# Optimization experiments

Measured on AMD Instinct MI355X. Metric: run time of the kernel, lower is better.

Reference implementation:

```python
import jax, jax.numpy as jnp
import numpy as np

B, M, D = 64, 256, 256          # batch, tokens, feature dim
A = 18                          # num_actions
E, S = 4, 64                    # num_experts, slots per expert (E*S == M)
H = 512                         # expert hidden size


def setup_inputs() -> dict:
    key = jax.random.key(0)
    ks = jax.random.split(key, 7)
    obs = jax.random.normal(ks[0], (B, M, D), dtype=jnp.float32)
    action = jax.random.randint(ks[1], (B,), 0, A, dtype=jnp.int64)
    # Soft-MoE slot projection phi: [D, E, S]
    phi = jax.random.normal(ks[2], (D, E, S), dtype=jnp.float32) / np.sqrt(D)
    # Per-expert MLP: Dense(H) + relu, then Dense(A*D) output head
    w1 = jax.random.normal(ks[3], (E, D, H), dtype=jnp.float32) * np.sqrt(2.0 / D)
    b1 = jnp.zeros((E, H), dtype=jnp.float32)
    w2 = jax.random.normal(ks[4], (E, H, A * D), dtype=jnp.float32) * np.sqrt(2.0 / H)
    b2 = jnp.zeros((E, A * D), dtype=jnp.float32)
    return {"obs": obs, "action": action, "phi": phi,
            "w1": w1, "b1": b1, "w2": w2, "b2": b2}


def reference(obs, action, phi, w1, b1, w2, b2):
    b, m, d = obs.shape
    # ---- Soft-MoE dispatch / combine (Puigcerver et al.) ----
    logits = jnp.einsum('bmd,des->bmes', obs, phi)            # [b,m,e,s]
    dispatch = jax.nn.softmax(logits, axis=1)                 # softmax over tokens
    combine = jax.nn.softmax(logits.reshape(b, m, E * S), axis=-1)
    combine = combine.reshape(b, m, E, S)                     # softmax over all slots
    slots = jnp.einsum('bmd,bmes->besd', obs, dispatch)       # [b,e,s,d]
    # ---- per-expert MLP: Dense(H)+relu -> Dense(A*d) ----
    h = jax.nn.relu(jnp.einsum('besd,edh->besh', slots, w1) + b1[None, :, None, :])
    y = jnp.einsum('besh,ehk->besk', h, w2) + b2[None, :, None, :]   # k = A*d
    # ---- combine slots back to tokens ----
    out = jnp.einsum('bmes,besk->bmk', combine, y)            # [b,m,A*d]
    # reshape to [b, A, m, d] as in the original module
    out = out.reshape(b, m, A, d).transpose(0, 2, 1, 3)       # [b,A,m,d]
    # ---- one-hot action selection via einsum (as in source) ----
    action_one_hot = jax.nn.one_hot(action, A, dtype=out.dtype)
    logits_out = jnp.einsum('bamd,ba->bmd', out, action_one_hot)
    return logits_out  # logits of the categorical transition distribution
```

## Files before the change

### kernel.cpp

```cpp
#include <hip/hip_runtime.h>

#define B_   64
#define M_   256
#define D_   256
#define A_   18
#define E_   4
#define S_   64
#define ES_  256
#define H_   512
#define K2_  (A_*D_)

typedef _Float16 f16;
typedef _Float16 f16x4 __attribute__((ext_vector_type(4)));
typedef _Float16 f16x8 __attribute__((ext_vector_type(8)));
typedef float    f32x4 __attribute__((ext_vector_type(4)));

static __device__ __forceinline__ f16x8 cat8(f16x4 a, f16x4 b) {
  return __builtin_shufflevector(a, b, 0, 1, 2, 3, 4, 5, 6, 7);
}
static __device__ __forceinline__ f16x8 pack8(float4 u0, float4 u1) {
  f16x8 a;
  a[0] = (f16)u0.x; a[1] = (f16)u0.y; a[2] = (f16)u0.z; a[3] = (f16)u0.w;
  a[4] = (f16)u1.x; a[5] = (f16)u1.y; a[6] = (f16)u1.z; a[7] = (f16)u1.w;
  return a;
}

typedef const __attribute__((address_space(1))) unsigned int guint;
typedef __attribute__((address_space(3))) unsigned int luint;
static __device__ __forceinline__ void gload16(const f16* g, f16* l) {
  __builtin_amdgcn_global_load_lds((guint*)g, (luint*)l, 16, 0, 0);
}

__global__ __launch_bounds__(256) void k_preplog(
    const float* __restrict__ obs, const float* __restrict__ phi,
    const float* __restrict__ w1, const float* __restrict__ w2,
    const int* __restrict__ action,
    f16* __restrict__ obsT16, f16* __restrict__ w1T, f16* __restrict__ w2T,
    int* __restrict__ order,
    f16* __restrict__ exp16, f16* __restrict__ expT16,
    float* __restrict__ rowpart, float* __restrict__ colpart)
{
  __shared__ f16 Bs[64][264];
  f16 (*T)[68] = reinterpret_cast<f16(*)[68]>(&Bs[0][0]);
  const int bx = blockIdx.x;
  const int t  = threadIdx.x;

  if (bx < 3456) {
    const int rr = t >> 4, cc = (t & 15) * 4;
    const float* src; f16* dst; int R, C, r0, c0;
    if (bx < 1024) {
      const int x = bx & 3, y = (bx >> 2) & 3, z = bx >> 4;
      src = obs + (long)z * (M_ * D_); dst = obsT16 + (long)z * (M_ * D_);
      R = M_; C = D_; r0 = y * 64; c0 = x * 64;
    } else if (bx < 1152) {
      const int idx = bx - 1024;
      const int x = idx & 7, y = (idx >> 3) & 3, z = idx >> 5;
      src = w1 + (long)z * (D_ * H_); dst = w1T + (long)z * (H_ * D_);
      R = D_; C = H_; r0 = y * 64; c0 = x * 64;
    } else {
      const int idx = bx - 1152;
      const int x = idx % 72, rem = idx / 72, y = rem & 7, z = rem >> 3;
      src = w2 + (long)z * ((long)H_ * K2_); dst = w2T + (long)z * ((long)K2_ * H_);
      R = H_; C = K2_; r0 = y * 64; c0 = x * 64;
    }
#pragma unroll
    for (int p = 0; p < 4; ++p) {
      const int row = rr + p * 16;
      const float4 v = *reinterpret_cast<const float4*>(
          &src[(long)(r0 + row) * C + c0 + cc]);
      T[row][cc + 0] = (f16)v.x; T[row][cc + 1] = (f16)v.y;
      T[row][cc + 2] = (f16)v.z; T[row][cc + 3] = (f16)v.w;
    }
    __syncthreads();
#pragma unroll
    for (int p = 0; p < 4; ++p) {
      const int oc = rr + p * 16;
      f16x4 g;
#pragma unroll
      for (int i = 0; i < 4; ++i) g[i] = T[cc + i][oc];
      *reinterpret_cast<f16x4*>(&dst[(long)(c0 + oc) * R + r0 + cc]) = g;
    }
    return;
  }

  if (bx == 3456) {
    if (t < B_) {
      const int a = action[t];
      int rank = 0;
#pragma unroll 8
      for (int i = 0; i < B_; ++i) {
        const int ai = action[i];
        rank += (ai < a) || (ai == a && i < t);
      }
      order[rank] = t;
    }
    return;
  }

  const int lb  = bx - 3457;
  const int es0 = (lb & 3) * 64, m0g = ((lb >> 2) & 3) * 64;
  const int bz  = lb >> 4;
  const long bo = (long)bz * (M_ * D_);
  const long bb = (long)bz * (M_ * ES_);

  {
    const int el = t & 63, wg = t >> 6;
#pragma unroll
    for (int dp = 0; dp < D_; dp += 32) {
      f16x8 hv;
#pragma unroll
      for (int j = 0; j < 8; ++j)
        hv[j] = (f16)phi[(long)(dp + wg * 8 + j) * ES_ + es0 + el];
      *reinterpret_cast<f16x8*>(&Bs[el][dp + wg * 8]) = hv;
    }
  }
  __syncthreads();

  const int w = t >> 6, lane = t & 63;
  const int wr = w >> 1, wc = w & 1;
  const int lr = lane & 15, lk = (lane >> 4) * 8;
  const int orow = (lane >> 4) * 4;

  f32x4 acc[2][2] = {};
  const float* Ap = obs + bo + (long)(m0g + wr * 32 + lr) * D_ + lk;
#pragma unroll
  for (int k0 = 0; k0 < D_; k0 += 32) {
    const float4 u00 = *reinterpret_cast<const float4*>(Ap + k0);
    const float4 u01 = *reinterpret_cast<const float4*>(Ap + k0 + 4);
    const float4 u10 = *reinterpret_cast<const float4*>(Ap + 16 * D_ + k0);
    const float4 u11 = *reinterpret_cast<const float4*>(Ap + 16 * D_ + k0 + 4);
    const f16x8 a0 = pack8(u00, u01);
    const f16x8 a1 = pack8(u10, u11);
    const f16x8 b0 = *reinterpret_cast<const f16x8*>(&Bs[wc * 32 + lr][k0 + lk]);
    const f16x8 b1 = *reinterpret_cast<const f16x8*>(&Bs[wc * 32 + 16 + lr][k0 + lk]);
    acc[0][0] = __builtin_amdgcn_mfma_f32_16x16x32_f16(a0, b0, acc[0][0], 0, 0, 0);
    acc[0][1] = __builtin_amdgcn_mfma_f32_16x16x32_f16(a0, b1, acc[0][1], 0, 0, 0);
    acc[1][0] = __builtin_amdgcn_mfma_f32_16x16x32_f16(a1, b0, acc[1][0], 0, 0, 0);
    acc[1][1] = __builtin_amdgcn_mfma_f32_16x16x32_f16(a1, b1, acc[1][1], 0, 0, 0);
  }
  __syncthreads();

#pragma unroll
  for (int fi = 0; fi < 2; ++fi)
#pragma unroll
    for (int fj = 0; fj < 2; ++fj) {
      const int gm = wr * 32 + fi * 16 + orow;
      const int gn = wc * 32 + fj * 16 + lr;
#pragma unroll
      for (int r = 0; r < 4; ++r)
        T[gm + r][gn] = (f16)__expf(acc[fi][fj][r]);
    }
  __syncthreads();

  {
    const int row = t >> 2, q = t & 3;
    f16x4 p0 = *reinterpret_cast<const f16x4*>(&T[row][q * 16 + 0]);
    f16x4 p1 = *reinterpret_cast<const f16x4*>(&T[row][q * 16 + 4]);
    f16x4 p2 = *reinterpret_cast<const f16x4*>(&T[row][q * 16 + 8]);
    f16x4 p3 = *reinterpret_cast<const f16x4*>(&T[row][q * 16 + 12]);
    f16* dst = exp16 + bb + (long)(m0g + row) * ES_ + es0 + q * 16;
    *reinterpret_cast<f16x8*>(dst)     = cat8(p0, p1);
    *reinterpret_cast<f16x8*>(dst + 8) = cat8(p2, p3);
  }
  {
    const int er = t >> 2, q = t & 3;
    f16x4 g[4];
#pragma unroll
    for (int j = 0; j < 4; ++j)
#pragma unroll
      for (int i = 0; i < 4; ++i)
        g[j][i] = T[q * 16 + j * 4 + i][er];
    f16* dst = expT16 + bb + (long)(es0 + er) * M_ + m0g + q * 16;
    *reinterpret_cast<f16x8*>(dst)     = cat8(g[0], g[1]);
    *reinterpret_cast<f16x8*>(dst + 8) = cat8(g[2], g[3]);
  }
  if (t < 64) {
    float s = 0.f;
#pragma unroll
    for (int i = 0; i < 16; ++i) {
      const f16x4 v = *reinterpret_cast<const f16x4*>(&T[t][i * 4]);
      s += (float)v[0] + (float)v[1] + (float)v[2] + (float)v[3];
    }
    rowpart[((long)bz * 256 + m0g + t) * 4 + (lb & 3)] = s;
  } else if (t < 128) {
    const int es = t - 64;
    float s = 0.f;
#pragma unroll
    for (int i = 0; i < 64; ++i) s += (float)T[i][es];
    colpart[((long)bz * 256 + es0 + es) * 4 + ((lb >> 2) & 3)] = s;
  }
}

#define SPAD 264
#define HPAD2 520
#define MFMA16(a, b, c) __builtin_amdgcn_mfma_f32_16x16x32_f16(a, b, c, 0, 0, 0)

__global__ __launch_bounds__(512, 4) void k_hy7(
    const f16* __restrict__ expT16, const f16* __restrict__ obsT16,
    const float* __restrict__ colpart,
    const f16* __restrict__ w1T, const float* __restrict__ b1,
    const f16* __restrict__ w2T, const float* __restrict__ b2,
    const int* __restrict__ action, const int* __restrict__ order,
    f16* __restrict__ yT16)
{
  __shared__ f16 ss[32][SPAD];
  __shared__ f16 hs[32][HPAD2];
  f16* ssL = &ss[0][0];
  f16* hsL = &hs[0][0];

  const int bx = blockIdx.x;
  const int L  = (bx & 7) * 64 + (bx >> 3);
  const int sb = L >> 3, e = (L >> 1) & 3, half = L & 1;
  const int b = order[sb];
  const int s0 = half * 32;
  int a = action[b];
  a = (a < 0) ? 0 : (a >= A_ ? A_ - 1 : a);

  const int t = threadIdx.x, w = t >> 6, lane = t & 63;
  const int lr = lane & 15, lk = (lane >> 4) * 8;
  const int seg = lane >> 4;
  const int orow = (lane >> 4) * 4;

  const f16* srcB0 = obsT16 + (long)b * (D_ * M_);
  const f16* srcB1 = w1T + (long)e * (H_ * D_);
  const f16* srcB2 = w2T + (long)e * ((long)K2_ * H_) + (long)a * D_ * H_;
  const f16* ApG0  = expT16 + (long)b * (ES_ * M_)
                   + (long)(e * S_ + s0 + lr) * M_ + lk;

  f32x4 acc00 = {}, acc01 = {}, acc10 = {}, acc11 = {};
#pragma unroll 1
  for (int kt = 0; kt < 8; ++kt) {
    __syncthreads();
#pragma unroll
    for (int p = 0; p < 2; ++p) {
      const int j = (w * 2 + p) * 64 + lane;
      const int row = j >> 2, sg = (j & 3) ^ (row & 3);
      gload16(srcB0 + (long)row * M_ + kt * 32 + sg * 8, ssL + (w * 2 + p) * 512);
    }
    __syncthreads();
    const f16x8 a0 = *reinterpret_cast<const f16x8*>(ApG0 + kt * 32);
    const f16x8 a1 = *reinterpret_cast<const f16x8*>(ApG0 + 16 * M_ + kt * 32);
    const int r0 = w * 32 + lr, r1 = w * 32 + 16 + lr;
    const f16x8 b0 = *reinterpret_cast<const f16x8*>(&ssL[r0 * 32 + ((seg ^ (r0 & 3)) * 8)]);
    const f16x8 b1 = *reinterpret_cast<const f16x8*>(&ssL[r1 * 32 + ((seg ^ (r1 & 3)) * 8)]);
    acc00 = MFMA16(a0, b0, acc00); acc01 = MFMA16(a0, b1, acc01);
    acc10 = MFMA16(a1, b0, acc10); acc11 = MFMA16(a1, b1, acc11);
  }
  __syncthreads();
  {
    f32x4 accs[2][2] = {{acc00, acc01}, {acc10, acc11}};
    const int n0 = w * 32;
#pragma unroll
    for (int fi = 0; fi < 2; ++fi) {
      float inv[4];
#pragma unroll
      for (int r = 0; r < 4; ++r) {
        const int ges = e * S_ + s0 + fi * 16 + orow + r;
        const float4 cp = *reinterpret_cast<const float4*>(
            &colpart[((long)b * 256 + ges) * 4]);
        inv[r] = 1.0f / (cp.x + cp.y + cp.z + cp.w);
      }
#pragma unroll
      for (int fj = 0; fj < 2; ++fj) {
        const int gm = fi * 16 + orow;
        const int gn = n0 + fj * 16 + lr;
#pragma unroll
        for (int r = 0; r < 4; ++r)
          ss[gm + r][gn] = (f16)(accs[fi][fj][r] * inv[r]);
      }
    }
  }
  __syncthreads();

  f32x4 g1acc[2][4] = {};
#pragma unroll 1
  for (int kt = 0; kt < 8; ++kt) {
    if (kt > 0) __syncthreads();
#pragma unroll
    for (int p = 0; p < 4; ++p) {
      const int j = (w * 4 + p) * 64 + lane;
      const int row = j >> 2, sg = (j & 3) ^ (row & 3);
      gload16(srcB1 + (long)row * D_ + kt * 32 + sg * 8, hsL + (w * 4 + p) * 512);
    }
    __syncthreads();
    f16x8 af[2];
    af[0] = *reinterpret_cast<const f16x8*>(&ss[lr][kt * 32 + lk]);
    af[1] = *reinterpret_cast<const f16x8*>(&ss[16 + lr][kt * 32 + lk]);
#pragma unroll
    for (int fj = 0; fj < 4; ++fj) {
      const int r = w * 64 + fj * 16 + lr;
      const f16x8 bf = *reinterpret_cast<const f16x8*>(&hsL[r * 32 + ((seg ^ (r & 3)) * 8)]);
      g1acc[0][fj] = MFMA16(af[0], bf, g1acc[0][fj]);
      g1acc[1][fj] = MFMA16(af[1], bf, g1acc[1][fj]);
    }
  }
  __syncthreads();

#pragma unroll
  for (int p = 0; p < 2; ++p) {
    const int j = (w * 2 + p) * 64 + lane;
    const int row = j >> 2, sg = (j & 3) ^ (row & 3);
    gload16(srcB2 + (long)row * H_ + sg * 8, ssL + (w * 2 + p) * 512);
  }
  {
    const int n1 = w * 64;
#pragma unroll
    for (int fi = 0; fi < 2; ++fi)
#pragma unroll
      for (int fj = 0; fj < 4; ++fj) {
        const int gm = fi * 16 + orow;
        const int gn = n1 + fj * 16 + lr;
        const float bv = b1[e * H_ + gn];
#pragma unroll
        for (int r = 0; r < 4; ++r)
          hs[gm + r][gn] = (f16)fmaxf(g1acc[fi][fj][r] + bv, 0.f);
      }
  }
  __syncthreads();

  f32x4 acc2[2][2] = {};
#pragma unroll 1
  for (int kt = 0; kt < 16; ++kt) {
    if (kt > 0) {
      __syncthreads();
#pragma unroll
      for (int p = 0; p < 2; ++p) {
        const int j = (w * 2 + p) * 64 + lane;
        const int row = j >> 2, sg = (j & 3) ^ (row & 3);
        gload16(srcB2 + (long)row * H_ + kt * 32 + sg * 8, ssL + (w * 2 + p) * 512);
      }
      __syncthreads();
    }
    f16x8 af[2];
    af[0] = *reinterpret_cast<const f16x8*>(&hs[lr][kt * 32 + lk]);
    af[1] = *reinterpret_cast<const f16x8*>(&hs[16 + lr][kt * 32 + lk]);
#pragma unroll
    for (int fj = 0; fj < 2; ++fj) {
      const int r = w * 32 + fj * 16 + lr;
      const f16x8 bf = *reinterpret_cast<const f16x8*>(&ssL[r * 32 + ((seg ^ (r & 3)) * 8)]);
      acc2[0][fj] = MFMA16(af[0], bf, acc2[0][fj]);
      acc2[1][fj] = MFMA16(af[1], bf, acc2[1][fj]);
    }
  }
  {
    const int n0_2 = w * 32;
#pragma unroll
    for (int fi = 0; fi < 2; ++fi)
#pragma unroll
      for (int fj = 0; fj < 2; ++fj) {
        const int gm = fi * 16 + orow;
        const int gn = n0_2 + fj * 16 + lr;
        const float bv = b2[e * K2_ + a * D_ + gn];
        f16x4 h4;
#pragma unroll
        for (int r = 0; r < 4; ++r) h4[r] = (f16)(acc2[fi][fj][r] + bv);
        *reinterpret_cast<f16x4*>(
            &yT16[(long)b * (D_ * ES_) + (long)gn * ES_ + e * S_ + s0 + gm]) = h4;
      }
  }
}

__global__ __launch_bounds__(256) void k_out_s(
    const f16* __restrict__ exp16, const f16* __restrict__ yT16,
    const float* __restrict__ rowpart, float* __restrict__ out)
{
  const int t = threadIdx.x;
  const int w = t >> 6, lane = t & 63;
  const int wr = w >> 1, wc = w & 1;
  const int m0 = blockIdx.y * 64 + wr * 32;
  const int n0 = blockIdx.x * 64 + wc * 32;
  const int lr = lane & 15, lk = (lane >> 4) * 8;
  const long b = blockIdx.z;

  f32x4 acc[2][2] = {};
  const f16* Ap = exp16 + b * (M_ * ES_) + (long)(m0 + lr) * ES_ + lk;
  const f16* Bp = yT16 + b * (D_ * ES_) + (long)(n0 + lr) * ES_ + lk;
#pragma unroll
  for (int k0 = 0; k0 < ES_; k0 += 32) {
    const f16x8 a0 = *reinterpret_cast<const f16x8*>(Ap + k0);
    const f16x8 a1 = *reinterpret_cast<const f16x8*>(Ap + 16 * ES_ + k0);
    const f16x8 b0 = *reinterpret_cast<const f16x8*>(Bp + k0);
    const f16x8 b1 = *reinterpret_cast<const f16x8*>(Bp + 16 * ES_ + k0);
    acc[0][0] = __builtin_amdgcn_mfma_f32_16x16x32_f16(a0, b0, acc[0][0], 0, 0, 0);
    acc[0][1] = __builtin_amdgcn_mfma_f32_16x16x32_f16(a0, b1, acc[0][1], 0, 0, 0);
    acc[1][0] = __builtin_amdgcn_mfma_f32_16x16x32_f16(a1, b0, acc[1][0], 0, 0, 0);
    acc[1][1] = __builtin_amdgcn_mfma_f32_16x16x32_f16(a1, b1, acc[1][1], 0, 0, 0);
  }

  const int orow = (lane >> 4) * 4;
  float* C = out + b * (M_ * D_);
#pragma unroll
  for (int fi = 0; fi < 2; ++fi) {
    float inv[4];
#pragma unroll
    for (int r = 0; r < 4; ++r) {
      const int gm = m0 + fi * 16 + orow + r;
      const float4 rp = *reinterpret_cast<const float4*>(&rowpart[((long)b * 256 + gm) * 4]);
      inv[r] = 1.0f / (rp.x + rp.y + rp.z + rp.w);
    }
#pragma unroll
    for (int fj = 0; fj < 2; ++fj) {
      const int gm = m0 + fi * 16 + orow;
      const int gn = n0 + fj * 16 + lr;
#pragma unroll
      for (int r = 0; r < 4; ++r)
        C[(long)(gm + r) * D_ + gn] = acc[fi][fj][r] * inv[r];
    }
  }
}

extern "C" void kernel_launch(void* const* d_in, const int* in_sizes, int n_in,
                              void* d_out, int out_size, void* d_ws, size_t ws_size,
                              hipStream_t stream)
{
  const float* obs    = (const float*)d_in[0];
  const int*   action = (const int*)d_in[1];
  const float* phi    = (const float*)d_in[2];
  const float* w1     = (const float*)d_in[3];
  const float* b1     = (const float*)d_in[4];
  const float* w2     = (const float*)d_in[5];
  const float* b2     = (const float*)d_in[6];
  float*       out    = (float*)d_out;

  f16* ws = (f16*)d_ws;
  f16* obsT16  = ws + 0;
  f16* w1T     = ws + 4194304;
  f16* w2T     = ws + 4718592;
  f16* exp16   = ws + 14155776;
  f16* expT16  = ws + 18350080;
  f16* yT16    = ws + 22544384;
  float* rowpart = (float*)(ws + 26738688);
  float* colpart = (float*)(ws + 26869760);
  int*   order   = (int*)(ws + 27000832);

  k_preplog<<<dim3(4481),     256, 0, stream>>>(obs, phi, w1, w2, action,
                                                obsT16, w1T, w2T, order,
                                                exp16, expT16, rowpart, colpart);
  k_hy7    <<<dim3(512),      512, 0, stream>>>(expT16, obsT16, colpart,
                                                w1T, b1, w2T, b2,
                                                action, order, yT16);
  k_out_s  <<<dim3(4, 4, 64), 256, 0, stream>>>(exp16, yT16, rowpart, out);
}
```

Measured before the change: 92.28 us.

## Double-buffer weight tiles in expert MLP kernel with explicit vmcnt waits

Rewrites the expert MLP kernel's two GEMM phases to double-buffer the w1 and w2 LDS tiles, prefetching tile k+2 while computing tile k. Plain __syncthreads are replaced with explicit s_waitcnt vmcnt, s_barrier and sched_barrier, so global-to-LDS loads overlap the MFMA work. The slot and hidden activations move to a single flat LDS buffer with XOR swizzling in place of padding. This raises LDS use to 80KB per block, which can lower occupancy against the launch bound of 4, and the hand-placed wait counts must match the load counts exactly.

```diff
diff --git a/kernel.cpp b/kernel.cpp
--- a/kernel.cpp
+++ b/kernel.cpp
@@ -30,6 +30,11 @@
 static __device__ __forceinline__ void gload16(const f16* g, f16* l) {
   __builtin_amdgcn_global_load_lds((guint*)g, (luint*)l, 16, 0, 0);
 }
+#define VMCNT(n)  asm volatile("s_waitcnt vmcnt(" #n ")" ::: "memory")
+#define LGKMCNT0  asm volatile("s_waitcnt lgkmcnt(0)" ::: "memory")
+#define SBAR()    __builtin_amdgcn_s_barrier()
+#define SCHED0()  __builtin_amdgcn_sched_barrier(0)
+#define MFMA16(a, b, c) __builtin_amdgcn_mfma_f32_16x16x32_f16(a, b, c, 0, 0, 0)
 
 __global__ __launch_bounds__(256) void k_preplog(
     const float* __restrict__ obs, const float* __restrict__ phi,
@@ -191,11 +196,7 @@
   }
 }
 
-#define SPAD 264
-#define HPAD2 520
-#define MFMA16(a, b, c) __builtin_amdgcn_mfma_f32_16x16x32_f16(a, b, c, 0, 0, 0)
-
-__global__ __launch_bounds__(512, 4) void k_hy7(
+__global__ __launch_bounds__(512, 4) void k_hy8(
     const f16* __restrict__ expT16, const f16* __restrict__ obsT16,
     const float* __restrict__ colpart,
     const f16* __restrict__ w1T, const float* __restrict__ b1,
@@ -203,10 +204,10 @@
     const int* __restrict__ action, const int* __restrict__ order,
     f16* __restrict__ yT16)
 {
-  __shared__ f16 ss[32][SPAD];
-  __shared__ f16 hs[32][HPAD2];
-  f16* ssL = &ss[0][0];
-  f16* hsL = &hs[0][0];
+  __shared__ f16 lds[40960];
+  f16* stg = lds;
+  f16* ssO = lds + 16384;
+  f16* hsO = lds + 24576;
 
   const int bx = blockIdx.x;
   const int L  = (bx & 7) * 64 + (bx >> 3);
@@ -220,6 +221,7 @@
   const int lr = lane & 15, lk = (lane >> 4) * 8;
   const int seg = lane >> 4;
   const int orow = (lane >> 4) * 4;
+  const int xorA = (lr & 7) << 3;
 
   const f16* srcB0 = obsT16 + (long)b * (D_ * M_);
   const f16* srcB1 = w1T + (long)e * (H_ * D_);
@@ -235,18 +237,25 @@
     for (int p = 0; p < 2; ++p) {
       const int j = (w * 2 + p) * 64 + lane;
       const int row = j >> 2, sg = (j & 3) ^ (row & 3);
-      gload16(srcB0 + (long)row * M_ + kt * 32 + sg * 8, ssL + (w * 2 + p) * 512);
+      gload16(srcB0 + (long)row * M_ + kt * 32 + sg * 8, stg + (w * 2 + p) * 512);
     }
     __syncthreads();
     const f16x8 a0 = *reinterpret_cast<const f16x8*>(ApG0 + kt * 32);
     const f16x8 a1 = *reinterpret_cast<const f16x8*>(ApG0 + 16 * M_ + kt * 32);
     const int r0 = w * 32 + lr, r1 = w * 32 + 16 + lr;
-    const f16x8 b0 = *reinterpret_cast<const f16x8*>(&ssL[r0 * 32 + ((seg ^ (r0 & 3)) * 8)]);
-    const f16x8 b1 = *reinterpret_cast<const f16x8*>(&ssL[r1 * 32 + ((seg ^ (r1 & 3)) * 8)]);
+    const f16x8 b0 = *reinterpret_cast<const f16x8*>(&stg[r0 * 32 + ((seg ^ (r0 & 3)) * 8)]);
+    const f16x8 b1 = *reinterpret_cast<const f16x8*>(&stg[r1 * 32 + ((seg ^ (r1 & 3)) * 8)]);
     acc00 = MFMA16(a0, b0, acc00); acc01 = MFMA16(a0, b1, acc01);
     acc10 = MFMA16(a1, b0, acc10); acc11 = MFMA16(a1, b1, acc11);
   }
   __syncthreads();
+
+#pragma unroll
+  for (int p = 0; p < 4; ++p) {
+    const int j = (w * 4 + p) * 64 + lane;
+    const int row = j >> 2, sg = (j & 3) ^ (row & 3);
+    gload16(srcB1 + (long)row * D_ + 0 * 32 + sg * 8, stg + (w * 4 + p) * 512);
+  }
   {
     f32x4 accs[2][2] = {{acc00, acc01}, {acc10, acc11}};
     const int n0 = w * 32;
@@ -262,45 +271,80 @@
       }
 #pragma unroll
       for (int fj = 0; fj < 2; ++fj) {
-        const int gm = fi * 16 + orow;
         const int gn = n0 + fj * 16 + lr;
 #pragma unroll
-        for (int r = 0; r < 4; ++r)
-          ss[gm + r][gn] = (f16)(accs[fi][fj][r] * inv[r]);
-      }
-    }
-  }
-  __syncthreads();
+        for (int r = 0; r < 4; ++r) {
+          const int row = fi * 16 + orow + r;
+          ssO[row * 256 + (gn ^ ((row & 7) << 3))] = (f16)(accs[fi][fj][r] * inv[r]);
+        }
+      }
+    }
+  }
+#pragma unroll
+  for (int p = 0; p < 4; ++p) {
+    const int j = (w * 4 + p) * 64 + lane;
+    const int row = j >> 2, sg = (j & 3) ^ (row & 3);
+    gload16(srcB1 + (long)row * D_ + 1 * 32 + sg * 8, hsO + (w * 4 + p) * 512);
+  }
+  LGKMCNT0; SBAR(); SCHED0();
 
   f32x4 g1acc[2][4] = {};
 #pragma unroll 1
-  for (int kt = 0; kt < 8; ++kt) {
-    if (kt > 0) __syncthreads();
-#pragma unroll
-    for (int p = 0; p < 4; ++p) {
-      const int j = (w * 4 + p) * 64 + lane;
-      const int row = j >> 2, sg = (j & 3) ^ (row & 3);
-      gload16(srcB1 + (long)row * D_ + kt * 32 + sg * 8, hsL + (w * 4 + p) * 512);
-    }
-    __syncthreads();
-    f16x8 af[2];
-    af[0] = *reinterpret_cast<const f16x8*>(&ss[lr][kt * 32 + lk]);
-    af[1] = *reinterpret_cast<const f16x8*>(&ss[16 + lr][kt * 32 + lk]);
+  for (int kt = 0; kt < 7; ++kt) {
+    VMCNT(4); SBAR(); SCHED0();
+    f16* buf = (kt & 1) ? hsO : stg;
+    {
+      const f16x8 af0 = *reinterpret_cast<const f16x8*>(
+          &ssO[lr * 256 + ((kt * 32 + lk) ^ xorA)]);
+      const f16x8 af1 = *reinterpret_cast<const f16x8*>(
+          &ssO[(16 + lr) * 256 + ((kt * 32 + lk) ^ xorA)]);
+#pragma unroll
+      for (int fj = 0; fj < 4; ++fj) {
+        const int rB = w * 64 + fj * 16 + lr;
+        const f16x8 bf = *reinterpret_cast<const f16x8*>(
+            &buf[rB * 32 + ((seg ^ (rB & 3)) * 8)]);
+        g1acc[0][fj] = MFMA16(af0, bf, g1acc[0][fj]);
+        g1acc[1][fj] = MFMA16(af1, bf, g1acc[1][fj]);
+      }
+    }
+    SBAR();
+    if (kt < 6) {
+#pragma unroll
+      for (int p = 0; p < 4; ++p) {
+        const int j = (w * 4 + p) * 64 + lane;
+        const int row = j >> 2, sg = (j & 3) ^ (row & 3);
+        gload16(srcB1 + (long)row * D_ + (kt + 2) * 32 + sg * 8, buf + (w * 4 + p) * 512);
+      }
+    }
+  }
+  VMCNT(0); SBAR(); SCHED0();
+  {
+    const f16x8 af0 = *reinterpret_cast<const f16x8*>(
+        &ssO[lr * 256 + ((7 * 32 + lk) ^ xorA)]);
+    const f16x8 af1 = *reinterpret_cast<const f16x8*>(
+        &ssO[(16 + lr) * 256 + ((7 * 32 + lk) ^ xorA)]);
 #pragma unroll
     for (int fj = 0; fj < 4; ++fj) {
-      const int r = w * 64 + fj * 16 + lr;
-      const f16x8 bf = *reinterpret_cast<const f16x8*>(&hsL[r * 32 + ((seg ^ (r & 3)) * 8)]);
-      g1acc[0][fj] = MFMA16(af[0], bf, g1acc[0][fj]);
-      g1acc[1][fj] = MFMA16(af[1], bf, g1acc[1][fj]);
-    }
-  }
-  __syncthreads();
+      const int rB = w * 64 + fj * 16 + lr;
+      const f16x8 bf = *reinterpret_cast<const f16x8*>(
+          &hsO[rB * 32 + ((seg ^ (rB & 3)) * 8)]);
+      g1acc[0][fj] = MFMA16(af0, bf, g1acc[0][fj]);
+      g1acc[1][fj] = MFMA16(af1, bf, g1acc[1][fj]);
+    }
+  }
+  SBAR();
 
 #pragma unroll
   for (int p = 0; p < 2; ++p) {
     const int j = (w * 2 + p) * 64 + lane;
     const int row = j >> 2, sg = (j & 3) ^ (row & 3);
-    gload16(srcB2 + (long)row * H_ + sg * 8, ssL + (w * 2 + p) * 512);
+    gload16(srcB2 + (long)row * H_ + 0 * 32 + sg * 8, stg + (w * 2 + p) * 512);
+  }
+#pragma unroll
+  for (int p = 0; p < 2; ++p) {
+    const int j = (w * 2 + p) * 64 + lane;
+    const int row = j >> 2, sg = (j & 3) ^ (row & 3);
+    gload16(srcB2 + (long)row * H_ + 1 * 32 + sg * 8, stg + 8192 + (w * 2 + p) * 512);
   }
   {
     const int n1 = w * 64;
@@ -308,38 +352,60 @@
     for (int fi = 0; fi < 2; ++fi)
 #pragma unroll
       for (int fj = 0; fj < 4; ++fj) {
-        const int gm = fi * 16 + orow;
         const int gn = n1 + fj * 16 + lr;
         const float bv = b1[e * H_ + gn];
 #pragma unroll
-        for (int r = 0; r < 4; ++r)
-          hs[gm + r][gn] = (f16)fmaxf(g1acc[fi][fj][r] + bv, 0.f);
-      }
-  }
-  __syncthreads();
+        for (int r = 0; r < 4; ++r) {
+          const int row = fi * 16 + orow + r;
+          hsO[row * 512 + (gn ^ ((row & 7) << 3))] =
+              (f16)fmaxf(g1acc[fi][fj][r] + bv, 0.f);
+        }
+      }
+  }
+  LGKMCNT0; SBAR(); SCHED0();
 
   f32x4 acc2[2][2] = {};
 #pragma unroll 1
-  for (int kt = 0; kt < 16; ++kt) {
-    if (kt > 0) {
-      __syncthreads();
+  for (int kt = 0; kt < 15; ++kt) {
+    VMCNT(2); SBAR(); SCHED0();
+    f16* buf = stg + (kt & 1) * 8192;
+    {
+      const f16x8 af0 = *reinterpret_cast<const f16x8*>(
+          &hsO[lr * 512 + ((kt * 32 + lk) ^ xorA)]);
+      const f16x8 af1 = *reinterpret_cast<const f16x8*>(
+          &hsO[(16 + lr) * 512 + ((kt * 32 + lk) ^ xorA)]);
+#pragma unroll
+      for (int fj = 0; fj < 2; ++fj) {
+        const int rB = w * 32 + fj * 16 + lr;
+        const f16x8 bf = *reinterpret_cast<const f16x8*>(
+            &buf[rB * 32 + ((seg ^ (rB & 3)) * 8)]);
+        acc2[0][fj] = MFMA16(af0, bf, acc2[0][fj]);
+        acc2[1][fj] = MFMA16(af1, bf, acc2[1][fj]);
+      }
+    }
+    SBAR();
+    if (kt < 14) {
 #pragma unroll
       for (int p = 0; p < 2; ++p) {
         const int j = (w * 2 + p) * 64 + lane;
         const int row = j >> 2, sg = (j & 3) ^ (row & 3);
-        gload16(srcB2 + (long)row * H_ + kt * 32 + sg * 8, ssL + (w * 2 + p) * 512);
-      }
-      __syncthreads();
-    }
-    f16x8 af[2];
-    af[0] = *reinterpret_cast<const f16x8*>(&hs[lr][kt * 32 + lk]);
-    af[1] = *reinterpret_cast<const f16x8*>(&hs[16 + lr][kt * 32 + lk]);
+        gload16(srcB2 + (long)row * H_ + (kt + 2) * 32 + sg * 8, buf + (w * 2 + p) * 512);
+      }
+    }
+  }
+  VMCNT(0); SBAR(); SCHED0();
+  {
+    const f16x8 af0 = *reinterpret_cast<const f16x8*>(
+        &hsO[lr * 512 + ((15 * 32 + lk) ^ xorA)]);
+    const f16x8 af1 = *reinterpret_cast<const f16x8*>(
+        &hsO[(16 + lr) * 512 + ((15 * 32 + lk) ^ xorA)]);
 #pragma unroll
     for (int fj = 0; fj < 2; ++fj) {
-      const int r = w * 32 + fj * 16 + lr;
-      const f16x8 bf = *reinterpret_cast<const f16x8*>(&ssL[r * 32 + ((seg ^ (r & 3)) * 8)]);
-      acc2[0][fj] = MFMA16(af[0], bf, acc2[0][fj]);
-      acc2[1][fj] = MFMA16(af[1], bf, acc2[1][fj]);
+      const int rB = w * 32 + fj * 16 + lr;
+      const f16x8 bf = *reinterpret_cast<const f16x8*>(
+          &stg[8192 + rB * 32 + ((seg ^ (rB & 3)) * 8)]);
+      acc2[0][fj] = MFMA16(af0, bf, acc2[0][fj]);
+      acc2[1][fj] = MFMA16(af1, bf, acc2[1][fj]);
     }
   }
   {
@@ -436,7 +502,7 @@
   k_preplog<<<dim3(4481),     256, 0, stream>>>(obs, phi, w1, w2, action,
                                                 obsT16, w1T, w2T, order,
                                                 exp16, expT16, rowpart, colpart);
-  k_hy7    <<<dim3(512),      512, 0, stream>>>(expT16, obsT16, colpart,
+  k_hy8    <<<dim3(512),      512, 0, stream>>>(expT16, obsT16, colpart,
                                                 w1T, b1, w2T, b2,
                                                 action, order, yT16);
   k_out_s  <<<dim3(4, 4, 64), 256, 0, stream>>>(exp16, yT16, rowpart, out);
```

Measured after the change: 89.66 us. -2.8%, faster.
